# Kernel tuning notes

Measured on AMD Instinct MI355X. Metric: run time of the kernel, lower is better.

Reference implementation:

```python
import jax, jax.numpy as jnp
import numpy as np

IN_V, OUT_V, IN_E = 64, 64, 64
B, N, E = 2, 1024, 8192


def setup_inputs() -> dict:
    key = jax.random.key(0)
    ks = jax.random.split(key, 8)
    return {
        "H_v": jax.random.normal(ks[0], (B * N, IN_V), dtype=jnp.float32),
        "H_e": jax.random.normal(ks[1], (B * E, IN_E), dtype=jnp.float32),
        "adj_e": jax.random.uniform(ks[2], (B * E, E), dtype=jnp.float32),
        "adj_v": jax.random.uniform(ks[3], (B * N, N), dtype=jnp.float32),
        "T": jax.random.uniform(ks[4], (B * N, E), dtype=jnp.float32),
        "weight": jax.random.normal(ks[5], (IN_V, OUT_V), dtype=jnp.float32) * (1.0 / np.sqrt(OUT_V)),
        "p": jax.random.normal(ks[6], (1, IN_E), dtype=jnp.float32),
        "bias": jax.random.normal(ks[7], (OUT_V,), dtype=jnp.float32) * (1.0 / np.sqrt(OUT_V)),
    }


def reference(H_v, H_e, adj_e, adj_v, T, weight, p, bias):
    # node_layer=True branch of AlternateConvolution
    b = adj_v.shape[0] // adj_v.shape[1]
    n = adj_v.shape[1]
    e = adj_e.shape[1]
    H_v = H_v.reshape(b, n, -1)            # [B,N,in_v]
    H_e = H_e.reshape(b, e, -1)            # [B,E,in_e]
    adj_v = adj_v.reshape(b, n, n)         # [B,N,N]
    T = T.reshape(b, n, e)                 # [B,N,E]
    # diag_embed(H_e @ p^T) then T @ diag @ T^T == row-scale T by (H_e @ p^T) then GEMM
    scale = jnp.einsum('bef,f->be', H_e, p[0])                  # [B,E]
    multiplier1 = jnp.einsum('bne,be,bme->bnm', T, scale, T)    # [B,N,N]
    eye = jnp.eye(n, dtype=bool)
    M1 = jnp.where(eye[None, :, :], jnp.ones_like(multiplier1), multiplier1)
    adjusted_A = M1 * adj_v
    output = jnp.einsum('bnm,bmd->bnd', adjusted_A, H_v @ weight) + bias
    return output, H_e
```

## Files before the change

### kernel.cpp

```cpp
#include <hip/hip_runtime.h>

#define Bb 2
#define Nn 1024
#define Ee 8192
#define DV 64

typedef __attribute__((ext_vector_type(8))) short short8;
typedef __attribute__((ext_vector_type(4))) float floatx4;

static __device__ __forceinline__ unsigned short f2bf(float f) {
    unsigned int u = __float_as_uint(f);
    unsigned int r = (u + 0x7FFFu + ((u >> 16) & 1u)) >> 16;
    return (unsigned short)r;
}

__global__ __launch_bounds__(256) void scale_kernel(const float* __restrict__ He,
                                                    const float* __restrict__ p,
                                                    float* __restrict__ scale) {
    int wave = threadIdx.x >> 6;
    int lane = threadIdx.x & 63;
    int row = blockIdx.x * 4 + wave;
    float v = He[row * 64 + lane] * p[lane];
    #pragma unroll
    for (int off = 32; off > 0; off >>= 1) v += __shfl_xor(v, off);
    if (lane == 0) scale[row] = v;
}

__global__ __launch_bounds__(256) void cast_kernel(const float* __restrict__ T,
                                                   const float* __restrict__ scale,
                                                   unsigned short* __restrict__ Tsc,
                                                   unsigned short* __restrict__ Tpl) {
    size_t i4 = (size_t)blockIdx.x * 256 + threadIdx.x;
    size_t e0 = i4 * 4;
    int b = (int)(e0 >> 23);
    int e = (int)(e0 & 8191);
    floatx4 t = *(const floatx4*)&T[e0];
    floatx4 s = *(const floatx4*)&scale[(size_t)b * Ee + e];
    ushort4 sc, pl;
    sc.x = f2bf(t.x * s.x); sc.y = f2bf(t.y * s.y);
    sc.z = f2bf(t.z * s.z); sc.w = f2bf(t.w * s.w);
    pl.x = f2bf(t.x); pl.y = f2bf(t.y);
    pl.z = f2bf(t.z); pl.w = f2bf(t.w);
    *(ushort4*)&Tsc[e0] = sc;
    *(ushort4*)&Tpl[e0] = pl;
}

__global__ __launch_bounds__(256) void hw_kernel(const float* __restrict__ Hv,
                                                 const float* __restrict__ W,
                                                 float* __restrict__ HWo) {
    __shared__ float Ws[64 * 64];
    __shared__ float Hvs[4 * 64];
    int t = threadIdx.x;
    for (int i = t; i < 4096; i += 256) Ws[i] = W[i];
    int r0 = blockIdx.x * 4;
    Hvs[t] = Hv[(size_t)r0 * 64 + t];
    __syncthreads();
    int d = t & 63, rr = t >> 6;
    float acc = 0.f;
    #pragma unroll
    for (int c = 0; c < 64; ++c) acc += Hvs[rr * 64 + c] * Ws[c * 64 + d];
    HWo[(size_t)(r0 + rr) * 64 + d] = acc;
}

__global__ __launch_bounds__(256, 2) void mm_kernel(const unsigned short* __restrict__ Tsc,
                                                    const unsigned short* __restrict__ Tpl,
                                                    float* __restrict__ Ppart) {
    __shared__ __attribute__((aligned(16))) unsigned short As[128 * 72];
    __shared__ __attribute__((aligned(16))) unsigned short Bs[128 * 72];
    const int t = threadIdx.x;
    const int tile = blockIdx.x;
    const int b = blockIdx.y;
    const int s = blockIdx.z;

    int i = 0, rem = tile;
    while (rem >= 8 - i) { rem -= 8 - i; ++i; }
    const int j = i + rem;
    const int n0 = i * 128, m0 = j * 128;

    const unsigned short* Arow = Tsc + ((size_t)b * Nn + n0) * Ee;
    const unsigned short* Brow = Tpl + ((size_t)b * Nn + m0) * Ee;

    const int kc0 = (s * 128) / 7 * 64;
    const int kc1 = ((s + 1) * 128) / 7 * 64;

    const int lane = t & 63;
    const int w = t >> 6;
    const int wr = w >> 1, wc = w & 1;
    const int quad = lane >> 4;
    const int l15 = lane & 15;

    const int r0s = t >> 3;
    const int c8 = t & 7;

    floatx4 acc[4][4];
    #pragma unroll
    for (int a = 0; a < 4; ++a)
        #pragma unroll
        for (int c = 0; c < 4; ++c) acc[a][c] = (floatx4){0.f, 0.f, 0.f, 0.f};

    for (int k0 = kc0; k0 < kc1; k0 += 64) {
        #pragma unroll
        for (int u = 0; u < 4; ++u) {
            int r = r0s + u * 32;
            short8 av = *(const short8*)&Arow[(size_t)r * Ee + k0 + c8 * 8];
            short8 bv = *(const short8*)&Brow[(size_t)r * Ee + k0 + c8 * 8];
            *(short8*)&As[r * 72 + c8 * 8] = av;
            *(short8*)&Bs[r * 72 + c8 * 8] = bv;
        }
        __syncthreads();
        #pragma unroll
        for (int kk = 0; kk < 64; kk += 32) {
            short8 af[4], bf[4];
            #pragma unroll
            for (int a = 0; a < 4; ++a)
                af[a] = *(const short8*)&As[(wr * 64 + a * 16 + l15) * 72 + kk + quad * 8];
            #pragma unroll
            for (int c = 0; c < 4; ++c)
                bf[c] = *(const short8*)&Bs[(wc * 64 + c * 16 + l15) * 72 + kk + quad * 8];
            #pragma unroll
            for (int a = 0; a < 4; ++a)
                #pragma unroll
                for (int c = 0; c < 4; ++c)
                    acc[a][c] = __builtin_amdgcn_mfma_f32_16x16x32_bf16(af[a], bf[c], acc[a][c], 0, 0, 0);
        }
        __syncthreads();
    }

    float* P = Ppart + (((size_t)(b * 36 + tile)) * 7 + s) * 16384;
    #pragma unroll
    for (int a = 0; a < 4; ++a)
        #pragma unroll
        for (int c = 0; c < 4; ++c)
            #pragma unroll
            for (int v = 0; v < 4; ++v) {
                int r = wr * 64 + a * 16 + quad * 4 + v;
                int cc = wc * 64 + c * 16 + l15;
                P[r * 128 + cc] = acc[a][c][v];
            }
}

__global__ __launch_bounds__(256) void reduce_kernel(const float* __restrict__ Ppart,
                                                     const float* __restrict__ adj_v,
                                                     float* __restrict__ Aout) {
    __shared__ float Ls[64 * 133];
    const int t = threadIdx.x;
    const int job = blockIdx.x;
    const int b = job / 36;
    const int tile = job % 36;
    int i = 0, rem = tile;
    while (rem >= 8 - i) { rem -= 8 - i; ++i; }
    const int j = i + rem;
    const int n0 = i * 128, m0 = j * 128;
    const float* P = Ppart + (size_t)job * 7 * 16384;
    const float* AV = adj_v + (size_t)b * Nn * Nn;
    float* AO = Aout + (size_t)b * Nn * Nn;

    for (int h = 0; h < 2; ++h) {
        #pragma unroll
        for (int it = 0; it < 8; ++it) {
            int f = it * 256 + t;
            int r = f >> 5;
            int c = (f & 31) * 4;
            floatx4 v = (floatx4){0.f, 0.f, 0.f, 0.f};
            #pragma unroll
            for (int s = 0; s < 7; ++s) {
                floatx4 pv = *(const floatx4*)&P[s * 16384 + (h * 64 + r) * 128 + c];
                v.x += pv.x; v.y += pv.y; v.z += pv.z; v.w += pv.w;
            }
            int gn = n0 + h * 64 + r;
            int gm = m0 + c;
            if (i == j) {
                if (gn == gm) v.x = 1.f;
                if (gn == gm + 1) v.y = 1.f;
                if (gn == gm + 2) v.z = 1.f;
                if (gn == gm + 3) v.w = 1.f;
            }
            Ls[r * 133 + c] = v.x; Ls[r * 133 + c + 1] = v.y;
            Ls[r * 133 + c + 2] = v.z; Ls[r * 133 + c + 3] = v.w;
            floatx4 a = *(const floatx4*)&AV[(size_t)gn * Nn + gm];
            floatx4 o = (floatx4){v.x * a.x, v.y * a.y, v.z * a.z, v.w * a.w};
            *(floatx4*)&AO[(size_t)gn * Nn + gm] = o;
        }
        __syncthreads();
        if (i != j) {
            #pragma unroll
            for (int it = 0; it < 8; ++it) {
                int f = it * 256 + t;
                int m = f >> 4;
                int cn = (f & 15) * 4;
                floatx4 v;
                v.x = Ls[(cn + 0) * 133 + m];
                v.y = Ls[(cn + 1) * 133 + m];
                v.z = Ls[(cn + 2) * 133 + m];
                v.w = Ls[(cn + 3) * 133 + m];
                int grow = m0 + m;
                int gcol = n0 + h * 64 + cn;
                floatx4 a = *(const floatx4*)&AV[(size_t)grow * Nn + gcol];
                floatx4 o = (floatx4){v.x * a.x, v.y * a.y, v.z * a.z, v.w * a.w};
                *(floatx4*)&AO[(size_t)grow * Nn + gcol] = o;
            }
        }
        __syncthreads();
    }
}

__global__ __launch_bounds__(256) void out_kernel(const float* __restrict__ A,
                                                  const float* __restrict__ HWo,
                                                  const float* __restrict__ bias,
                                                  float* __restrict__ out) {
    __shared__ float HWs[64 * 64];
    __shared__ float Ash[8 * 64];
    int t = threadIdx.x;
    int b = blockIdx.y;
    int n0 = blockIdx.x * 8;
    int d = t & 63;
    int rr = t >> 6;
    float acc0 = 0.f, acc1 = 0.f;
    for (int m0 = 0; m0 < Nn; m0 += 64) {
        for (int i = t; i < 4096; i += 256) {
            int r = i >> 6, c = i & 63;
            HWs[i] = HWo[((size_t)b * Nn + m0 + r) * 64 + c];
        }
        {
            int i = t;
            int r = i >> 6, c = i & 63;
            Ash[i] = A[((size_t)b * Nn + n0 + r) * Nn + m0 + c];
            i += 256; r = i >> 6; c = i & 63;
            Ash[i] = A[((size_t)b * Nn + n0 + r) * Nn + m0 + c];
        }
        __syncthreads();
        #pragma unroll
        for (int mm = 0; mm < 64; ++mm) {
            float hw = HWs[mm * 64 + d];
            acc0 += Ash[rr * 64 + mm] * hw;
            acc1 += Ash[(rr + 4) * 64 + mm] * hw;
        }
        __syncthreads();
    }
    float bd = bias[d];
    out[((size_t)b * Nn + n0 + rr) * 64 + d] = acc0 + bd;
    out[((size_t)b * Nn + n0 + rr + 4) * 64 + d] = acc1 + bd;
}

extern "C" void kernel_launch(void* const* d_in, const int* in_sizes, int n_in,
                              void* d_out, int out_size, void* d_ws, size_t ws_size,
                              hipStream_t stream) {
    const float* H_v    = (const float*)d_in[0];
    const float* H_e    = (const float*)d_in[1];
    const float* adj_v  = (const float*)d_in[3];
    const float* T      = (const float*)d_in[4];
    const float* weight = (const float*)d_in[5];
    const float* p      = (const float*)d_in[6];
    const float* bias   = (const float*)d_in[7];
    float* out = (float*)d_out;

    char* ws = (char*)d_ws;
    float* scale          = (float*)ws;
    float* HWo            = (float*)(ws + (1 << 16));
    unsigned short* Tsc   = (unsigned short*)(ws + (1 << 20));
    unsigned short* Tpl   = (unsigned short*)(ws + (1 << 20) + (32u << 20));
    float* Ppart          = (float*)(ws + (1 << 20) + (64u << 20));
    float* Aout           = (float*)(ws + (1 << 20) + (98u << 20));

    hipMemcpyAsync(out + (size_t)Bb * Nn * DV, H_e,
                   (size_t)Bb * Ee * 64 * sizeof(float),
                   hipMemcpyDeviceToDevice, stream);

    scale_kernel<<<dim3(Bb * Ee / 4), dim3(256), 0, stream>>>(H_e, p, scale);
    cast_kernel<<<dim3((Bb * Nn * Ee / 4) / 256), dim3(256), 0, stream>>>(T, scale, Tsc, Tpl);
    hw_kernel<<<dim3(Bb * Nn / 4), dim3(256), 0, stream>>>(H_v, weight, HWo);
    mm_kernel<<<dim3(36, Bb, 7), dim3(256), 0, stream>>>(Tsc, Tpl, Ppart);
    reduce_kernel<<<dim3(36 * Bb), dim3(256), 0, stream>>>(Ppart, adj_v, Aout);
    out_kernel<<<dim3(Nn / 8, Bb), dim3(256), 0, stream>>>(Aout, HWo, bias, out);
}
```

Measured before the change: 726.5 us.

## Use direct global-to-LDS loads with XOR swizzle in GEMM; split reduce over halves

The GEMM tile staging now uses global_load_lds to copy T tiles straight into shared memory, skipping the register round-trip. The shared layout changes from padded rows to an unpadded XOR-swizzled layout to avoid bank conflicts. The reduce kernel's two half-tile passes are split across a second grid dimension, doubling the number of blocks. The direct-to-LDS builtin relies on each wave writing a contiguous LDS span, so the per-lane mapping has to match that wave layout exactly.

```diff
diff --git a/kernel.cpp b/kernel.cpp
--- a/kernel.cpp
+++ b/kernel.cpp
@@ -65,8 +65,8 @@
 __global__ __launch_bounds__(256, 2) void mm_kernel(const unsigned short* __restrict__ Tsc,
                                                     const unsigned short* __restrict__ Tpl,
                                                     float* __restrict__ Ppart) {
-    __shared__ __attribute__((aligned(16))) unsigned short As[128 * 72];
-    __shared__ __attribute__((aligned(16))) unsigned short Bs[128 * 72];
+    __shared__ __attribute__((aligned(16))) unsigned short As[128 * 64];
+    __shared__ __attribute__((aligned(16))) unsigned short Bs[128 * 64];
     const int t = threadIdx.x;
     const int tile = blockIdx.x;
     const int b = blockIdx.y;
@@ -76,21 +76,24 @@
     while (rem >= 8 - i) { rem -= 8 - i; ++i; }
     const int j = i + rem;
     const int n0 = i * 128, m0 = j * 128;
-
-    const unsigned short* Arow = Tsc + ((size_t)b * Nn + n0) * Ee;
-    const unsigned short* Brow = Tpl + ((size_t)b * Nn + m0) * Ee;
-
-    const int kc0 = (s * 128) / 7 * 64;
-    const int kc1 = ((s + 1) * 128) / 7 * 64;
 
     const int lane = t & 63;
     const int w = t >> 6;
     const int wr = w >> 1, wc = w & 1;
     const int quad = lane >> 4;
     const int l15 = lane & 15;
-
-    const int r0s = t >> 3;
-    const int c8 = t & 7;
+    const int l7 = l15 & 7;
+
+    const int lr = lane >> 3;
+    const int lc = (lane & 7) ^ lr;
+
+    const int kc0 = (s * 128) / 7 * 64;
+    const int kc1 = ((s + 1) * 128) / 7 * 64;
+
+    const unsigned short* gA = Tsc + ((size_t)b * Nn + n0 + w * 32 + lr) * Ee + kc0 + lc * 8;
+    const unsigned short* gB = Tpl + ((size_t)b * Nn + m0 + w * 32 + lr) * Ee + kc0 + lc * 8;
+    unsigned short* lA = As + (w * 32) * 64 + lane * 8;
+    unsigned short* lB = Bs + (w * 32) * 64 + lane * 8;
 
     floatx4 acc[4][4];
     #pragma unroll
@@ -101,22 +104,24 @@
     for (int k0 = kc0; k0 < kc1; k0 += 64) {
         #pragma unroll
         for (int u = 0; u < 4; ++u) {
-            int r = r0s + u * 32;
-            short8 av = *(const short8*)&Arow[(size_t)r * Ee + k0 + c8 * 8];
-            short8 bv = *(const short8*)&Brow[(size_t)r * Ee + k0 + c8 * 8];
-            *(short8*)&As[r * 72 + c8 * 8] = av;
-            *(short8*)&Bs[r * 72 + c8 * 8] = bv;
-        }
-        __syncthreads();
-        #pragma unroll
-        for (int kk = 0; kk < 64; kk += 32) {
+            __builtin_amdgcn_global_load_lds(
+                (const __attribute__((address_space(1))) unsigned int*)(gA + (size_t)u * 8 * Ee),
+                (__attribute__((address_space(3))) unsigned int*)(lA + u * 8 * 64), 16, 0, 0);
+            __builtin_amdgcn_global_load_lds(
+                (const __attribute__((address_space(1))) unsigned int*)(gB + (size_t)u * 8 * Ee),
+                (__attribute__((address_space(3))) unsigned int*)(lB + u * 8 * 64), 16, 0, 0);
+        }
+        gA += 64; gB += 64;
+        __syncthreads();
+        #pragma unroll
+        for (int kk8 = 0; kk8 < 8; kk8 += 4) {
             short8 af[4], bf[4];
             #pragma unroll
             for (int a = 0; a < 4; ++a)
-                af[a] = *(const short8*)&As[(wr * 64 + a * 16 + l15) * 72 + kk + quad * 8];
+                af[a] = *(const short8*)&As[(wr * 64 + a * 16 + l15) * 64 + ((kk8 + quad) ^ l7) * 8];
             #pragma unroll
             for (int c = 0; c < 4; ++c)
-                bf[c] = *(const short8*)&Bs[(wc * 64 + c * 16 + l15) * 72 + kk + quad * 8];
+                bf[c] = *(const short8*)&Bs[(wc * 64 + c * 16 + l15) * 64 + ((kk8 + quad) ^ l7) * 8];
             #pragma unroll
             for (int a = 0; a < 4; ++a)
                 #pragma unroll
@@ -145,6 +150,7 @@
     __shared__ float Ls[64 * 133];
     const int t = threadIdx.x;
     const int job = blockIdx.x;
+    const int h = blockIdx.y;
     const int b = job / 36;
     const int tile = job % 36;
     int i = 0, rem = tile;
@@ -155,52 +161,49 @@
     const float* AV = adj_v + (size_t)b * Nn * Nn;
     float* AO = Aout + (size_t)b * Nn * Nn;
 
-    for (int h = 0; h < 2; ++h) {
+    #pragma unroll
+    for (int it = 0; it < 8; ++it) {
+        int f = it * 256 + t;
+        int r = f >> 5;
+        int c = (f & 31) * 4;
+        floatx4 v = (floatx4){0.f, 0.f, 0.f, 0.f};
+        #pragma unroll
+        for (int s = 0; s < 7; ++s) {
+            floatx4 pv = *(const floatx4*)&P[s * 16384 + (h * 64 + r) * 128 + c];
+            v.x += pv.x; v.y += pv.y; v.z += pv.z; v.w += pv.w;
+        }
+        int gn = n0 + h * 64 + r;
+        int gm = m0 + c;
+        if (i == j) {
+            if (gn == gm) v.x = 1.f;
+            if (gn == gm + 1) v.y = 1.f;
+            if (gn == gm + 2) v.z = 1.f;
+            if (gn == gm + 3) v.w = 1.f;
+        }
+        Ls[r * 133 + c] = v.x; Ls[r * 133 + c + 1] = v.y;
+        Ls[r * 133 + c + 2] = v.z; Ls[r * 133 + c + 3] = v.w;
+        floatx4 a = *(const floatx4*)&AV[(size_t)gn * Nn + gm];
+        floatx4 o = (floatx4){v.x * a.x, v.y * a.y, v.z * a.z, v.w * a.w};
+        *(floatx4*)&AO[(size_t)gn * Nn + gm] = o;
+    }
+    __syncthreads();
+    if (i != j) {
         #pragma unroll
         for (int it = 0; it < 8; ++it) {
             int f = it * 256 + t;
-            int r = f >> 5;
-            int c = (f & 31) * 4;
-            floatx4 v = (floatx4){0.f, 0.f, 0.f, 0.f};
-            #pragma unroll
-            for (int s = 0; s < 7; ++s) {
-                floatx4 pv = *(const floatx4*)&P[s * 16384 + (h * 64 + r) * 128 + c];
-                v.x += pv.x; v.y += pv.y; v.z += pv.z; v.w += pv.w;
-            }
-            int gn = n0 + h * 64 + r;
-            int gm = m0 + c;
-            if (i == j) {
-                if (gn == gm) v.x = 1.f;
-                if (gn == gm + 1) v.y = 1.f;
-                if (gn == gm + 2) v.z = 1.f;
-                if (gn == gm + 3) v.w = 1.f;
-            }
-            Ls[r * 133 + c] = v.x; Ls[r * 133 + c + 1] = v.y;
-            Ls[r * 133 + c + 2] = v.z; Ls[r * 133 + c + 3] = v.w;
-            floatx4 a = *(const floatx4*)&AV[(size_t)gn * Nn + gm];
+            int m = f >> 4;
+            int cn = (f & 15) * 4;
+            floatx4 v;
+            v.x = Ls[(cn + 0) * 133 + m];
+            v.y = Ls[(cn + 1) * 133 + m];
+            v.z = Ls[(cn + 2) * 133 + m];
+            v.w = Ls[(cn + 3) * 133 + m];
+            int grow = m0 + m;
+            int gcol = n0 + h * 64 + cn;
+            floatx4 a = *(const floatx4*)&AV[(size_t)grow * Nn + gcol];
             floatx4 o = (floatx4){v.x * a.x, v.y * a.y, v.z * a.z, v.w * a.w};
-            *(floatx4*)&AO[(size_t)gn * Nn + gm] = o;
-        }
-        __syncthreads();
-        if (i != j) {
-            #pragma unroll
-            for (int it = 0; it < 8; ++it) {
-                int f = it * 256 + t;
-                int m = f >> 4;
-                int cn = (f & 15) * 4;
-                floatx4 v;
-                v.x = Ls[(cn + 0) * 133 + m];
-                v.y = Ls[(cn + 1) * 133 + m];
-                v.z = Ls[(cn + 2) * 133 + m];
-                v.w = Ls[(cn + 3) * 133 + m];
-                int grow = m0 + m;
-                int gcol = n0 + h * 64 + cn;
-                floatx4 a = *(const floatx4*)&AV[(size_t)grow * Nn + gcol];
-                floatx4 o = (floatx4){v.x * a.x, v.y * a.y, v.z * a.z, v.w * a.w};
-                *(floatx4*)&AO[(size_t)grow * Nn + gcol] = o;
-            }
-        }
-        __syncthreads();
+            *(floatx4*)&AO[(size_t)grow * Nn + gcol] = o;
+        }
     }
 }
 
@@ -270,6 +273,6 @@
     cast_kernel<<<dim3((Bb * Nn * Ee / 4) / 256), dim3(256), 0, stream>>>(T, scale, Tsc, Tpl);
     hw_kernel<<<dim3(Bb * Nn / 4), dim3(256), 0, stream>>>(H_v, weight, HWo);
     mm_kernel<<<dim3(36, Bb, 7), dim3(256), 0, stream>>>(Tsc, Tpl, Ppart);
-    reduce_kernel<<<dim3(36 * Bb), dim3(256), 0, stream>>>(Ppart, adj_v, Aout);
+    reduce_kernel<<<dim3(36 * Bb, 2), dim3(256), 0, stream>>>(Ppart, adj_v, Aout);
     out_kernel<<<dim3(Nn / 8, Bb), dim3(256), 0, stream>>>(Aout, HWo, bias, out);
 }
```

New measurement: 714.1 us. About the same (-1.7%).
